# Performance work log

Measured on AMD Instinct MI355X. Metric: run time of the kernel, lower is better.

The kernel has to match this reference:

```python
import jax, jax.numpy as jnp
import numpy as np

N_NODES = 20000
N_GRAPH = 256
NODE_DIM = 128
MULS = (128, 64, 32)       # node irreps: 128x0e + 64x1o + 32x2e
HC = 32                    # hidden channels per irrep
HIDDEN_DIM = 64
N_PATH = 9                 # feasible uuw paths into 0e+1e+2e
W_NUMEL = N_PATH * HC * HC # 9216


def _tables():
    # real Clebsch-Gordan tensors built from cartesian tensor algebra,
    # normalized so that sum(C**2) = 2*l_out + 1 (component normalization)
    eps = np.zeros((3, 3, 3))
    eps[0, 1, 2] = eps[1, 2, 0] = eps[2, 0, 1] = 1.0
    eps[0, 2, 1] = eps[2, 1, 0] = eps[1, 0, 2] = -1.0
    s2, s6 = 1 / np.sqrt(2), 1 / np.sqrt(6)
    Q2 = np.zeros((5, 3, 3))  # orthonormal basis of traceless symmetric 3x3
    Q2[0, 0, 1] = Q2[0, 1, 0] = s2          # xy
    Q2[1, 1, 2] = Q2[1, 2, 1] = s2          # yz
    Q2[2, 0, 0] = Q2[2, 1, 1] = -s6; Q2[2, 2, 2] = 2 * s6  # z2
    Q2[3, 0, 2] = Q2[3, 2, 0] = s2          # xz
    Q2[4, 0, 0] = s2; Q2[4, 1, 1] = -s2     # x2-y2

    def nrm(C, l3):
        return C * np.sqrt((2 * l3 + 1) / (C ** 2).sum())

    C000 = np.ones((1, 1, 1))
    C022 = np.eye(5)[None, :, :]
    C110 = np.eye(3).reshape(3, 3, 1) / np.sqrt(3)
    C111 = eps / np.sqrt(2)
    C112 = np.transpose(Q2, (1, 2, 0))
    C202 = np.eye(5)[:, None, :]
    C220 = np.eye(5).reshape(5, 5, 1) / np.sqrt(5)
    M = np.einsum('iab,jdb->ijad', Q2, Q2)  # [5,5,3,3]
    C221 = nrm(np.einsum('cad,ijad->ijc', eps, M), 1)
    S = 0.5 * (M + np.transpose(M, (0, 1, 3, 2)))
    S = S - np.trace(S, axis1=2, axis2=3)[..., None, None] * np.eye(3) / 3.0
    C222 = nrm(np.einsum('kad,ijad->ijk', Q2, S), 2)
    # sph2cart change of basis: 9 spherical comps (0e+1e+2e) -> 3x3 cartesian
    Qc = np.zeros((3, 3, 9))
    Qc[:, :, 0] = np.eye(3) / np.sqrt(3)        # isotropic part
    Qc[:, :, 1:4] = eps / np.sqrt(2)            # antisymmetric part
    Qc[:, :, 4:9] = np.transpose(Q2, (1, 2, 0)) # symmetric traceless part
    return [C000, C022, C110, C111, C112, C202, C220, C221, C222], Qc

_CGS, _QC = _tables()


def setup_inputs() -> dict:
    key = jax.random.key(0)
    ks = jax.random.split(key, 12)
    f32 = jnp.float32
    d_sph = MULS[0] + 3 * MULS[1] + 5 * MULS[2]  # 480
    return {
        'x_scalar': jax.random.normal(ks[0], (N_NODES, NODE_DIM), f32),
        'x_spherical': jax.random.normal(ks[1], (N_NODES, d_sph), f32),
        'batch': jnp.sort(jax.random.randint(ks[2], (N_NODES,), 0, N_GRAPH)),
        'W0e': jax.random.normal(ks[3], (MULS[0], HC), f32),
        'W1o': jax.random.normal(ks[4], (MULS[1], HC), f32),
        'W2e': jax.random.normal(ks[5], (MULS[2], HC), f32),
        'Wm1': jax.random.normal(ks[6], (NODE_DIM, HIDDEN_DIM), f32) / np.sqrt(NODE_DIM),
        'bm1': jnp.zeros((HIDDEN_DIM,), f32),
        'Wm2': jax.random.normal(ks[7], (HIDDEN_DIM, W_NUMEL), f32) / np.sqrt(HIDDEN_DIM),
        'bm2': jnp.zeros((W_NUMEL,), f32),
        'P0': jax.random.normal(ks[8], (3 * HC,), f32),
        'P1': jax.random.normal(ks[9], (2 * HC,), f32),
        'P2': jax.random.normal(ks[10], (4 * HC,), f32),
    }


def reference(x_scalar, x_spherical, batch, W0e, W1o, W2e, Wm1, bm1, Wm2, bm2, P0, P1, P2):
    n = x_scalar.shape[0]
    m0, m1, m2 = MULS
    # split node features into irrep blocks
    x0 = x_spherical[:, :m0, None]                        # [N,128,1] 0e
    x1 = x_spherical[:, m0:m0 + 3 * m1].reshape(n, m1, 3) # [N,64,3]  1o
    x2 = x_spherical[:, m0 + 3 * m1:].reshape(n, m2, 5)   # [N,32,5]  2e
    # pre_lin: per-irrep channel mixing (e3nn-style 1/sqrt(fan_in))
    h = [jnp.einsum('num,uv->nvm', x, W) / np.sqrt(W.shape[0])
         for x, W in ((x0, W0e), (x1, W1o), (x2, W2e))]   # each [N,32,2l+1]
    # per-node tensor-product weights from scalar features
    w = (jax.nn.silu(x_scalar @ Wm1 + bm1) @ Wm2 + bm2).reshape(n, N_PATH, HC, HC)
    # uuw tensor product, path order matches _CGS
    paths = ((0, 0), (0, 2), (1, 1), (1, 1), (1, 1), (2, 0), (2, 2), (2, 2), (2, 2))
    inv_u = 1.0 / np.sqrt(HC)
    outs = []
    for k, (i, j) in enumerate(paths):
        C = jnp.asarray(_CGS[k], x_scalar.dtype)
        outs.append(jnp.einsum('pqr,nup,nuq,nuw->nwr', C, h[i], h[j], w[:, k]) * inv_u)
    # post_lin: combine paths of each output l into a single channel
    y0 = jnp.einsum('num,u->nm', jnp.concatenate([outs[0], outs[2], outs[6]], 1), P0) / np.sqrt(3 * HC)
    y1 = jnp.einsum('num,u->nm', jnp.concatenate([outs[3], outs[7]], 1), P1) / np.sqrt(2 * HC)
    y2 = jnp.einsum('num,u->nm', jnp.concatenate([outs[1], outs[4], outs[5], outs[8]], 1), P2) / np.sqrt(4 * HC)
    sph = jnp.concatenate([y0, y1, y2], axis=1)           # [N,9]
    cart = jnp.einsum('abi,ni->nab', jnp.asarray(_QC, sph.dtype), sph)  # [N,3,3]
    red = jax.ops.segment_sum(cart, batch, num_segments=N_GRAPH)        # [B,3,3]
    # if_trace is False (if_iso=False): roll every non-batch dim by 1
    return jnp.roll(jnp.roll(red, 1, axis=1), 1, axis=2)
```

## Files before the change

### kernel.cpp

```cpp
#include <hip/hip_runtime.h>
#include <math.h>

#define OFF_W2P 0
#define OFF_B2P 14336
#define OFF_V   14592
#define OFF_H0  4494592
#define OFF_H1  5134592
#define OFF_H2  7054592
#define WS_FLOATS 10254592

#define SC_Y0 0.0180421959121758f
#define SC_Y2 0.015625f
#define S2f 0.70710678118654752f
#define S6f 0.40824829046386302f
#define TWOS2f 1.41421356237309505f
#define TWOS6f 0.81649658092772603f
#define ISQRT3 0.57735026918962576f
#define ISQRT5 0.44721359549995794f
#define H0SC 0.08838834764831845f
#define H1SC 0.125f
#define H2SC 0.17677669529663689f

__device__ __constant__ int KARR[7] = {0, 1, 2, 4, 5, 6, 8};

__global__ __launch_bounds__(256) void prep_kernel(
    const float* __restrict__ Wm2, const float* __restrict__ bm2,
    const float* __restrict__ P0, const float* __restrict__ P2,
    float* __restrict__ ws, float* __restrict__ out) {
  int j = blockIdx.x * 256 + threadIdx.x;
  if (j < 2304) out[j] = 0.f;

  if (j < 14336) {
    int s = j >> 11; int rem = j & 2047; int c = rem >> 5; int u = rem & 31;
    int k = KARR[s];
    const float* P;
    float sc;
    switch (s) {
      case 0: P = P0;      sc = SC_Y0; break;
      case 1: P = P2;      sc = SC_Y2; break;
      case 2: P = P0 + 32; sc = SC_Y0; break;
      case 3: P = P2 + 32; sc = SC_Y2; break;
      case 4: P = P2 + 64; sc = SC_Y2; break;
      case 5: P = P0 + 64; sc = SC_Y0; break;
      default: P = P2 + 96; sc = SC_Y2; break;
    }
    const float4* w4 = (const float4*)(Wm2 + c * 9216 + k * 1024 + u * 32);
    const float4* p4 = (const float4*)P;
    float acc = 0.f;
#pragma unroll
    for (int q = 0; q < 8; ++q) {
      float4 a = w4[q], b = p4[q];
      acc += a.x * b.x + a.y * b.y + a.z * b.z + a.w * b.w;
    }
    ws[OFF_W2P + c * 224 + s * 32 + u] = acc * sc;
  } else if (j < 14560) {
    int i = j - 14336; int s = i >> 5; int u = i & 31; int k = KARR[s];
    const float* P;
    float sc;
    switch (s) {
      case 0: P = P0;      sc = SC_Y0; break;
      case 1: P = P2;      sc = SC_Y2; break;
      case 2: P = P0 + 32; sc = SC_Y0; break;
      case 3: P = P2 + 32; sc = SC_Y2; break;
      case 4: P = P2 + 64; sc = SC_Y2; break;
      case 5: P = P0 + 64; sc = SC_Y0; break;
      default: P = P2 + 96; sc = SC_Y2; break;
    }
    const float* b = bm2 + k * 1024 + u * 32;
    float acc = 0.f;
#pragma unroll
    for (int w = 0; w < 32; ++w) acc += b[w] * P[w];
    ws[OFF_B2P + s * 32 + u] = acc * sc;
  }
}

__global__ __launch_bounds__(256, 1) void kbc_kernel(
    const float* __restrict__ xs_g, const float* __restrict__ xsph,
    const float* __restrict__ W0e, const float* __restrict__ W1o,
    const float* __restrict__ W2e,
    const float* __restrict__ Wm1, const float* __restrict__ bm1,
    float* __restrict__ ws) {
  __shared__ __align__(16) char smem[30976];
  const int tid = threadIdx.x;

  if (blockIdx.x < 625) {
    float (*xs)[132] = (float (*)[132])smem;
    float (*hiT)[36] = (float (*)[36])(smem + 16896);
    const int n0 = blockIdx.x * 32;

    for (int idx = tid; idx < 1024; idx += 256) {
      const int row = idx >> 5, c4 = idx & 31;
      *(float4*)&xs[row][c4 * 4] = *(const float4*)(xs_g + (n0 + row) * 128 + c4 * 4);
    }
    __syncthreads();

    {
      const int cg = tid & 15, ng = tid >> 4;
      const int c0 = cg * 4, nl = ng * 2;
      float acc[2][4] = {{0.f}};
#pragma unroll 4
      for (int mq = 0; mq < 32; ++mq) {
        float4 xv[2];
        xv[0] = *(float4*)&xs[nl][mq * 4];
        xv[1] = *(float4*)&xs[nl + 1][mq * 4];
        float4 wv[4];
#pragma unroll
        for (int r = 0; r < 4; ++r) wv[r] = *(const float4*)(Wm1 + (mq * 4 + r) * 64 + c0);
#pragma unroll
        for (int r = 0; r < 4; ++r) {
          const float4 w = wv[r];
#pragma unroll
          for (int i = 0; i < 2; ++i) {
            const float xr = (r == 0) ? xv[i].x : (r == 1) ? xv[i].y : (r == 2) ? xv[i].z : xv[i].w;
            acc[i][0] += xr * w.x; acc[i][1] += xr * w.y;
            acc[i][2] += xr * w.z; acc[i][3] += xr * w.w;
          }
        }
      }
      const float4 bb = *(const float4*)(bm1 + c0);
#pragma unroll
      for (int jj = 0; jj < 4; ++jj) {
        float zz[2];
#pragma unroll
        for (int i = 0; i < 2; ++i) {
          float z = acc[i][jj] + ((jj == 0) ? bb.x : (jj == 1) ? bb.y : (jj == 2) ? bb.z : bb.w);
          zz[i] = z / (1.f + __expf(-z));
        }
        *(float2*)&hiT[c0 + jj][nl] = make_float2(zz[0], zz[1]);
      }
    }
    __syncthreads();

    if (tid < 224) {
      const int og = tid >> 3, ng = tid & 7;
      const int o0 = og * 8, nl = ng * 4;
      const float4 blo = *(const float4*)(ws + OFF_B2P + o0);
      const float4 bhi = *(const float4*)(ws + OFF_B2P + o0 + 4);
      float acc[4][8];
#pragma unroll
      for (int i = 0; i < 4; ++i) {
        acc[i][0] = blo.x; acc[i][1] = blo.y; acc[i][2] = blo.z; acc[i][3] = blo.w;
        acc[i][4] = bhi.x; acc[i][5] = bhi.y; acc[i][6] = bhi.z; acc[i][7] = bhi.w;
      }
#pragma unroll 2
      for (int c = 0; c < 64; ++c) {
        const float4 hv = *(float4*)&hiT[c][nl];
        const float4 wlo = *(const float4*)(ws + OFF_W2P + c * 224 + o0);
        const float4 whi = *(const float4*)(ws + OFF_W2P + c * 224 + o0 + 4);
        const float hvv[4] = {hv.x, hv.y, hv.z, hv.w};
        const float wv[8] = {wlo.x, wlo.y, wlo.z, wlo.w, whi.x, whi.y, whi.z, whi.w};
#pragma unroll
        for (int i = 0; i < 4; ++i)
#pragma unroll
          for (int jj = 0; jj < 8; ++jj) acc[i][jj] += hvv[i] * wv[jj];
      }
#pragma unroll
      for (int i = 0; i < 4; ++i) {
        const int n = n0 + nl + i;
        float4 a = {acc[i][0], acc[i][1], acc[i][2], acc[i][3]};
        float4 b = {acc[i][4], acc[i][5], acc[i][6], acc[i][7]};
        *(float4*)(ws + OFF_V + n * 224 + o0) = a;
        *(float4*)(ws + OFF_V + n * 224 + o0 + 4) = b;
      }
    }
  } else {
    float (*xp)[484] = (float (*)[484])smem;
    const int n0 = (blockIdx.x - 625) * 16;

    for (int idx = tid; idx < 1920; idx += 256) {
      const int row = idx / 120, c4 = idx % 120;
      *(float4*)&xp[row][c4 * 4] = *(const float4*)(xsph + (size_t)(n0 + row) * 480 + c4 * 4);
    }
    __syncthreads();

    if (tid < 64) {
      const int n = tid & 15, ug = tid >> 4;
      const int u0 = ug * 8;
      float acc[8] = {0.f};
#pragma unroll 4
      for (int mq = 0; mq < 32; ++mq) {
        const float4 xv = *(float4*)&xp[n][mq * 4];
        const float xa[4] = {xv.x, xv.y, xv.z, xv.w};
#pragma unroll
        for (int r = 0; r < 4; ++r) {
          const float4 wl = *(const float4*)(W0e + (mq * 4 + r) * 32 + u0);
          const float4 wh = *(const float4*)(W0e + (mq * 4 + r) * 32 + u0 + 4);
          const float xr = xa[r];
          acc[0] += xr * wl.x; acc[1] += xr * wl.y; acc[2] += xr * wl.z; acc[3] += xr * wl.w;
          acc[4] += xr * wh.x; acc[5] += xr * wh.y; acc[6] += xr * wh.z; acc[7] += xr * wh.w;
        }
      }
      const int n_g = n0 + n;
      float4 a = {acc[0] * H0SC, acc[1] * H0SC, acc[2] * H0SC, acc[3] * H0SC};
      float4 b = {acc[4] * H0SC, acc[5] * H0SC, acc[6] * H0SC, acc[7] * H0SC};
      *(float4*)(ws + OFF_H0 + n_g * 32 + u0) = a;
      *(float4*)(ws + OFF_H0 + n_g * 32 + u0 + 4) = b;
    } else if (tid < 128) {
      const int t = tid - 64;
      const int n = t & 15, ug = t >> 4;
      const int u0 = ug * 8;
      float acc[3][8] = {{0.f}};
#pragma unroll 2
      for (int mq = 0; mq < 16; ++mq) {
        const float4 a0 = *(float4*)&xp[n][128 + mq * 12];
        const float4 a1 = *(float4*)&xp[n][128 + mq * 12 + 4];
        const float4 a2 = *(float4*)&xp[n][128 + mq * 12 + 8];
        const float xa[12] = {a0.x, a0.y, a0.z, a0.w, a1.x, a1.y, a1.z, a1.w,
                              a2.x, a2.y, a2.z, a2.w};
#pragma unroll
        for (int mm = 0; mm < 4; ++mm) {
          const float4 wl = *(const float4*)(W1o + (mq * 4 + mm) * 32 + u0);
          const float4 wh = *(const float4*)(W1o + (mq * 4 + mm) * 32 + u0 + 4);
          const float wv[8] = {wl.x, wl.y, wl.z, wl.w, wh.x, wh.y, wh.z, wh.w};
#pragma unroll
          for (int j = 0; j < 3; ++j) {
            const float xr = xa[mm * 3 + j];
#pragma unroll
            for (int jj = 0; jj < 8; ++jj) acc[j][jj] += xr * wv[jj];
          }
        }
      }
      const int n_g = n0 + n;
#pragma unroll
      for (int j = 0; j < 3; ++j) {
        float4 a = {acc[j][0] * H1SC, acc[j][1] * H1SC, acc[j][2] * H1SC, acc[j][3] * H1SC};
        float4 b = {acc[j][4] * H1SC, acc[j][5] * H1SC, acc[j][6] * H1SC, acc[j][7] * H1SC};
        *(float4*)(ws + OFF_H1 + (n_g * 3 + j) * 32 + u0) = a;
        *(float4*)(ws + OFF_H1 + (n_g * 3 + j) * 32 + u0 + 4) = b;
      }
    } else if (tid < 192) {
      const int t = tid - 128;
      const int n = t & 15, ug = t >> 4;
      const int u0 = ug * 8;
      float acc[5][8] = {{0.f}};
#pragma unroll 2
      for (int mq = 0; mq < 8; ++mq) {
        const float4 a0 = *(float4*)&xp[n][320 + mq * 20];
        const float4 a1 = *(float4*)&xp[n][320 + mq * 20 + 4];
        const float4 a2 = *(float4*)&xp[n][320 + mq * 20 + 8];
        const float4 a3 = *(float4*)&xp[n][320 + mq * 20 + 12];
        const float4 a4 = *(float4*)&xp[n][320 + mq * 20 + 16];
        const float xa[20] = {a0.x, a0.y, a0.z, a0.w, a1.x, a1.y, a1.z, a1.w,
                              a2.x, a2.y, a2.z, a2.w, a3.x, a3.y, a3.z, a3.w,
                              a4.x, a4.y, a4.z, a4.w};
#pragma unroll
        for (int mm = 0; mm < 4; ++mm) {
          const float4 wl = *(const float4*)(W2e + (mq * 4 + mm) * 32 + u0);
          const float4 wh = *(const float4*)(W2e + (mq * 4 + mm) * 32 + u0 + 4);
          const float wv[8] = {wl.x, wl.y, wl.z, wl.w, wh.x, wh.y, wh.z, wh.w};
#pragma unroll
          for (int j = 0; j < 5; ++j) {
            const float xr = xa[mm * 5 + j];
#pragma unroll
            for (int jj = 0; jj < 8; ++jj) acc[j][jj] += xr * wv[jj];
          }
        }
      }
      const int n_g = n0 + n;
#pragma unroll
      for (int j = 0; j < 5; ++j) {
        float4 a = {acc[j][0] * H2SC, acc[j][1] * H2SC, acc[j][2] * H2SC, acc[j][3] * H2SC};
        float4 b = {acc[j][4] * H2SC, acc[j][5] * H2SC, acc[j][6] * H2SC, acc[j][7] * H2SC};
        *(float4*)(ws + OFF_H2 + (n_g * 5 + j) * 32 + u0) = a;
        *(float4*)(ws + OFF_H2 + (n_g * 5 + j) * 32 + u0 + 4) = b;
      }
    }
  }
}

__global__ __launch_bounds__(256) void kd_kernel(
    const float* __restrict__ ws, const int* __restrict__ batch,
    float* __restrict__ out, const float norm2) {
  const int tid = threadIdx.x;
  const int nl = tid >> 5, un = tid & 31;
  const int n0 = blockIdx.x * 8;
  const int n = n0 + nl;

  const float* V = ws + OFF_V + n * 224 + un;
  const float v0 = V[0], v1 = V[32], v2 = V[64], v3 = V[96];
  const float v4 = V[128], v5 = V[160], v6 = V[192];
  const float h0 = ws[OFF_H0 + n * 32 + un];
  const float h1a = ws[OFF_H1 + (n * 3 + 0) * 32 + un];
  const float h1b = ws[OFF_H1 + (n * 3 + 1) * 32 + un];
  const float h1c = ws[OFF_H1 + (n * 3 + 2) * 32 + un];
  float h2v[5];
#pragma unroll
  for (int j = 0; j < 5; ++j) h2v[j] = ws[OFF_H2 + (n * 5 + j) * 32 + un];

  const float d11 = h1a * h1a + h1b * h1b + h1c * h1c;
  const float d22 = h2v[0] * h2v[0] + h2v[1] * h2v[1] + h2v[2] * h2v[2] +
                    h2v[3] * h2v[3] + h2v[4] * h2v[4];
  float y0 = v0 * h0 * h0 + v2 * d11 * ISQRT3 + v5 * d22 * ISQRT5;

  const float o00 = h1a * h1a, o01 = h1a * h1b, o02 = h1a * h1c;
  const float o11 = h1b * h1b, o12 = h1b * h1c, o22 = h1c * h1c;
  const float t40 = TWOS2f * o01, t41 = TWOS2f * o12;
  const float t42 = S6f * (2.f * o22 - o00 - o11);
  const float t43 = TWOS2f * o02, t44 = S2f * (o00 - o11);

  const float A00 = -S6f * h2v[2] + S2f * h2v[4];
  const float A01 = S2f * h2v[0];
  const float A02 = S2f * h2v[3];
  const float A11 = -S6f * h2v[2] - S2f * h2v[4];
  const float A12 = S2f * h2v[1];
  const float A22 = TWOS6f * h2v[2];
  const float B00 = A00 * A00 + A01 * A01 + A02 * A02;
  const float B01 = A00 * A01 + A01 * A11 + A02 * A12;
  const float B02 = A00 * A02 + A01 * A12 + A02 * A22;
  const float B11 = A01 * A01 + A11 * A11 + A12 * A12;
  const float B12 = A01 * A02 + A11 * A12 + A12 * A22;
  const float B22 = A02 * A02 + A12 * A12 + A22 * A22;
  const float t80 = TWOS2f * B01, t81 = TWOS2f * B12;
  const float t82 = S6f * (2.f * B22 - B00 - B11);
  const float t83 = TWOS2f * B02, t84 = S2f * (B00 - B11);

  const float w15 = (v1 + v4) * h0;
  const float v6n = v6 * norm2;
  float y2r[5];
  y2r[0] = w15 * h2v[0] + v3 * t40 + v6n * t80;
  y2r[1] = w15 * h2v[1] + v3 * t41 + v6n * t81;
  y2r[2] = w15 * h2v[2] + v3 * t42 + v6n * t82;
  y2r[3] = w15 * h2v[3] + v3 * t43 + v6n * t83;
  y2r[4] = w15 * h2v[4] + v3 * t44 + v6n * t84;

#pragma unroll
  for (int off = 16; off > 0; off >>= 1) {
    y0 += __shfl_xor(y0, off, 32);
#pragma unroll
    for (int r = 0; r < 5; ++r) y2r[r] += __shfl_xor(y2r[r], off, 32);
  }

  __shared__ float sphs[8][6];
  if (un == 0) {
    sphs[nl][0] = y0;
#pragma unroll
    for (int r = 0; r < 5; ++r) sphs[nl][1 + r] = y2r[r];
  }
  __syncthreads();

  if (tid < 9) {
    const float QW[9][6] = {
        {ISQRT3, 0.f, 0.f, -S6f, 0.f, S2f},
        {0.f, S2f, 0.f, 0.f, 0.f, 0.f},
        {0.f, 0.f, 0.f, 0.f, S2f, 0.f},
        {0.f, S2f, 0.f, 0.f, 0.f, 0.f},
        {ISQRT3, 0.f, 0.f, -S6f, 0.f, -S2f},
        {0.f, 0.f, S2f, 0.f, 0.f, 0.f},
        {0.f, 0.f, 0.f, 0.f, S2f, 0.f},
        {0.f, 0.f, S2f, 0.f, 0.f, 0.f},
        {ISQRT3, 0.f, 0.f, TWOS6f, 0.f, 0.f}};
    const int a = tid / 3, b = tid % 3;
    const int rolled = ((a + 1) % 3) * 3 + ((b + 1) % 3);
    const float c0 = QW[tid][0], c1 = QW[tid][1], c2 = QW[tid][2];
    const float c3 = QW[tid][3], c4 = QW[tid][4], c5 = QW[tid][5];
    int cur_g = batch[n0];
    float acc = 0.f;
#pragma unroll
    for (int q = 0; q < 8; ++q) {
      const int g = batch[n0 + q];
      const float val = c0 * sphs[q][0] + c1 * sphs[q][1] + c2 * sphs[q][2] +
                        c3 * sphs[q][3] + c4 * sphs[q][4] + c5 * sphs[q][5];
      if (g != cur_g) {
        atomicAdd(out + cur_g * 9 + rolled, acc);
        acc = 0.f;
        cur_g = g;
      }
      acc += val;
    }
    atomicAdd(out + cur_g * 9 + rolled, acc);
  }
}

extern "C" void kernel_launch(void* const* d_in, const int* in_sizes, int n_in,
                              void* d_out, int out_size, void* d_ws, size_t ws_size,
                              hipStream_t stream) {
  const float* x_scalar = (const float*)d_in[0];
  const float* x_sph    = (const float*)d_in[1];
  const int*   batch    = (const int*)d_in[2];
  const float* W0e      = (const float*)d_in[3];
  const float* W1o      = (const float*)d_in[4];
  const float* W2e      = (const float*)d_in[5];
  const float* Wm1      = (const float*)d_in[6];
  const float* bm1      = (const float*)d_in[7];
  const float* Wm2      = (const float*)d_in[8];
  const float* bm2      = (const float*)d_in[9];
  const float* P0       = (const float*)d_in[10];
  const float* P2       = (const float*)d_in[12];
  float* ws  = (float*)d_ws;
  float* out = (float*)d_out;

  if (ws_size < (size_t)WS_FLOATS * sizeof(float)) return;

  double Q2[5][3][3] = {};
  const double s2d = 0.70710678118654752440, s6d = 0.40824829046386301637;
  Q2[0][0][1] = Q2[0][1][0] = s2d;
  Q2[1][1][2] = Q2[1][2][1] = s2d;
  Q2[2][0][0] = Q2[2][1][1] = -s6d; Q2[2][2][2] = 2.0 * s6d;
  Q2[3][0][2] = Q2[3][2][0] = s2d;
  Q2[4][0][0] = s2d; Q2[4][1][1] = -s2d;
  double ss = 0.0;
  for (int i = 0; i < 5; ++i)
    for (int jj = 0; jj < 5; ++jj) {
      double S[3][3];
      for (int a = 0; a < 3; ++a)
        for (int d = 0; d < 3; ++d) {
          double m1 = 0, m2 = 0;
          for (int b = 0; b < 3; ++b) {
            m1 += Q2[i][a][b] * Q2[jj][d][b];
            m2 += Q2[i][d][b] * Q2[jj][a][b];
          }
          S[a][d] = 0.5 * (m1 + m2);
        }
      double tr = (S[0][0] + S[1][1] + S[2][2]) / 3.0;
      S[0][0] -= tr; S[1][1] -= tr; S[2][2] -= tr;
      for (int kk = 0; kk < 5; ++kk) {
        double cc = 0;
        for (int a = 0; a < 3; ++a)
          for (int d = 0; d < 3; ++d) cc += Q2[kk][a][d] * S[a][d];
        ss += cc * cc;
      }
    }
  const float norm2 = (float)sqrt(5.0 / ss);

  prep_kernel<<<57, 256, 0, stream>>>(Wm2, bm2, P0, P2, ws, out);
  kbc_kernel<<<1875, 256, 0, stream>>>(x_scalar, x_sph, W0e, W1o, W2e, Wm1, bm1, ws);
  kd_kernel<<<2500, 256, 0, stream>>>(ws, batch, out, norm2);
}
```

Baseline: 157.0 us.

## Fuse projection, weight MLP and tensor-product reduction into one kernel

Merges the node-projection/MLP kernel and the tensor-product/segment-sum kernel into a single kernel that processes 16 nodes per block. The per-node V, h0, h1 and h2 intermediates now stay in shared memory and registers instead of being written to and re-read from a large global workspace. This removes that HBM round trip and one kernel launch. In exchange each block uses about 50 KB of shared memory and must do all stages serially, and the work per stage is split differently across threads (e.g. one output channel per thread for the h projections), which may lower per-stage efficiency or occupancy.

```diff
diff --git a/kernel.cpp b/kernel.cpp
--- a/kernel.cpp
+++ b/kernel.cpp
@@ -3,11 +3,7 @@
 
 #define OFF_W2P 0
 #define OFF_B2P 14336
-#define OFF_V   14592
-#define OFF_H0  4494592
-#define OFF_H1  5134592
-#define OFF_H2  7054592
-#define WS_FLOATS 10254592
+#define WS_FLOATS 14592
 
 #define SC_Y0 0.0180421959121758f
 #define SC_Y2 0.015625f
@@ -74,267 +70,227 @@
   }
 }
 
-__global__ __launch_bounds__(256, 1) void kbc_kernel(
+__global__ __launch_bounds__(256, 3) void fused_kernel(
     const float* __restrict__ xs_g, const float* __restrict__ xsph,
     const float* __restrict__ W0e, const float* __restrict__ W1o,
     const float* __restrict__ W2e,
     const float* __restrict__ Wm1, const float* __restrict__ bm1,
-    float* __restrict__ ws) {
-  __shared__ __align__(16) char smem[30976];
-  const int tid = threadIdx.x;
-
-  if (blockIdx.x < 625) {
-    float (*xs)[132] = (float (*)[132])smem;
-    float (*hiT)[36] = (float (*)[36])(smem + 16896);
-    const int n0 = blockIdx.x * 32;
-
-    for (int idx = tid; idx < 1024; idx += 256) {
-      const int row = idx >> 5, c4 = idx & 31;
-      *(float4*)&xs[row][c4 * 4] = *(const float4*)(xs_g + (n0 + row) * 128 + c4 * 4);
-    }
-    __syncthreads();
-
-    {
-      const int cg = tid & 15, ng = tid >> 4;
-      const int c0 = cg * 4, nl = ng * 2;
-      float acc[2][4] = {{0.f}};
-#pragma unroll 4
-      for (int mq = 0; mq < 32; ++mq) {
-        float4 xv[2];
-        xv[0] = *(float4*)&xs[nl][mq * 4];
-        xv[1] = *(float4*)&xs[nl + 1][mq * 4];
-        float4 wv[4];
-#pragma unroll
-        for (int r = 0; r < 4; ++r) wv[r] = *(const float4*)(Wm1 + (mq * 4 + r) * 64 + c0);
-#pragma unroll
-        for (int r = 0; r < 4; ++r) {
-          const float4 w = wv[r];
-#pragma unroll
-          for (int i = 0; i < 2; ++i) {
-            const float xr = (r == 0) ? xv[i].x : (r == 1) ? xv[i].y : (r == 2) ? xv[i].z : xv[i].w;
-            acc[i][0] += xr * w.x; acc[i][1] += xr * w.y;
-            acc[i][2] += xr * w.z; acc[i][3] += xr * w.w;
-          }
-        }
-      }
-      const float4 bb = *(const float4*)(bm1 + c0);
-#pragma unroll
-      for (int jj = 0; jj < 4; ++jj) {
-        float zz[2];
-#pragma unroll
-        for (int i = 0; i < 2; ++i) {
-          float z = acc[i][jj] + ((jj == 0) ? bb.x : (jj == 1) ? bb.y : (jj == 2) ? bb.z : bb.w);
-          zz[i] = z / (1.f + __expf(-z));
-        }
-        *(float2*)&hiT[c0 + jj][nl] = make_float2(zz[0], zz[1]);
-      }
-    }
-    __syncthreads();
-
-    if (tid < 224) {
-      const int og = tid >> 3, ng = tid & 7;
-      const int o0 = og * 8, nl = ng * 4;
-      const float4 blo = *(const float4*)(ws + OFF_B2P + o0);
-      const float4 bhi = *(const float4*)(ws + OFF_B2P + o0 + 4);
-      float acc[4][8];
-#pragma unroll
-      for (int i = 0; i < 4; ++i) {
-        acc[i][0] = blo.x; acc[i][1] = blo.y; acc[i][2] = blo.z; acc[i][3] = blo.w;
-        acc[i][4] = bhi.x; acc[i][5] = bhi.y; acc[i][6] = bhi.z; acc[i][7] = bhi.w;
-      }
-#pragma unroll 2
-      for (int c = 0; c < 64; ++c) {
-        const float4 hv = *(float4*)&hiT[c][nl];
-        const float4 wlo = *(const float4*)(ws + OFF_W2P + c * 224 + o0);
-        const float4 whi = *(const float4*)(ws + OFF_W2P + c * 224 + o0 + 4);
-        const float hvv[4] = {hv.x, hv.y, hv.z, hv.w};
-        const float wv[8] = {wlo.x, wlo.y, wlo.z, wlo.w, whi.x, whi.y, whi.z, whi.w};
-#pragma unroll
-        for (int i = 0; i < 4; ++i)
-#pragma unroll
-          for (int jj = 0; jj < 8; ++jj) acc[i][jj] += hvv[i] * wv[jj];
-      }
-#pragma unroll
-      for (int i = 0; i < 4; ++i) {
-        const int n = n0 + nl + i;
-        float4 a = {acc[i][0], acc[i][1], acc[i][2], acc[i][3]};
-        float4 b = {acc[i][4], acc[i][5], acc[i][6], acc[i][7]};
-        *(float4*)(ws + OFF_V + n * 224 + o0) = a;
-        *(float4*)(ws + OFF_V + n * 224 + o0 + 4) = b;
-      }
-    }
-  } else {
-    float (*xp)[484] = (float (*)[484])smem;
-    const int n0 = (blockIdx.x - 625) * 16;
-
-    for (int idx = tid; idx < 1920; idx += 256) {
-      const int row = idx / 120, c4 = idx % 120;
-      *(float4*)&xp[row][c4 * 4] = *(const float4*)(xsph + (size_t)(n0 + row) * 480 + c4 * 4);
-    }
-    __syncthreads();
-
-    if (tid < 64) {
-      const int n = tid & 15, ug = tid >> 4;
-      const int u0 = ug * 8;
-      float acc[8] = {0.f};
-#pragma unroll 4
-      for (int mq = 0; mq < 32; ++mq) {
-        const float4 xv = *(float4*)&xp[n][mq * 4];
-        const float xa[4] = {xv.x, xv.y, xv.z, xv.w};
-#pragma unroll
-        for (int r = 0; r < 4; ++r) {
-          const float4 wl = *(const float4*)(W0e + (mq * 4 + r) * 32 + u0);
-          const float4 wh = *(const float4*)(W0e + (mq * 4 + r) * 32 + u0 + 4);
-          const float xr = xa[r];
-          acc[0] += xr * wl.x; acc[1] += xr * wl.y; acc[2] += xr * wl.z; acc[3] += xr * wl.w;
-          acc[4] += xr * wh.x; acc[5] += xr * wh.y; acc[6] += xr * wh.z; acc[7] += xr * wh.w;
-        }
-      }
-      const int n_g = n0 + n;
-      float4 a = {acc[0] * H0SC, acc[1] * H0SC, acc[2] * H0SC, acc[3] * H0SC};
-      float4 b = {acc[4] * H0SC, acc[5] * H0SC, acc[6] * H0SC, acc[7] * H0SC};
-      *(float4*)(ws + OFF_H0 + n_g * 32 + u0) = a;
-      *(float4*)(ws + OFF_H0 + n_g * 32 + u0 + 4) = b;
-    } else if (tid < 128) {
-      const int t = tid - 64;
-      const int n = t & 15, ug = t >> 4;
-      const int u0 = ug * 8;
-      float acc[3][8] = {{0.f}};
-#pragma unroll 2
-      for (int mq = 0; mq < 16; ++mq) {
-        const float4 a0 = *(float4*)&xp[n][128 + mq * 12];
-        const float4 a1 = *(float4*)&xp[n][128 + mq * 12 + 4];
-        const float4 a2 = *(float4*)&xp[n][128 + mq * 12 + 8];
-        const float xa[12] = {a0.x, a0.y, a0.z, a0.w, a1.x, a1.y, a1.z, a1.w,
-                              a2.x, a2.y, a2.z, a2.w};
-#pragma unroll
-        for (int mm = 0; mm < 4; ++mm) {
-          const float4 wl = *(const float4*)(W1o + (mq * 4 + mm) * 32 + u0);
-          const float4 wh = *(const float4*)(W1o + (mq * 4 + mm) * 32 + u0 + 4);
-          const float wv[8] = {wl.x, wl.y, wl.z, wl.w, wh.x, wh.y, wh.z, wh.w};
-#pragma unroll
-          for (int j = 0; j < 3; ++j) {
-            const float xr = xa[mm * 3 + j];
-#pragma unroll
-            for (int jj = 0; jj < 8; ++jj) acc[j][jj] += xr * wv[jj];
-          }
-        }
-      }
-      const int n_g = n0 + n;
-#pragma unroll
-      for (int j = 0; j < 3; ++j) {
-        float4 a = {acc[j][0] * H1SC, acc[j][1] * H1SC, acc[j][2] * H1SC, acc[j][3] * H1SC};
-        float4 b = {acc[j][4] * H1SC, acc[j][5] * H1SC, acc[j][6] * H1SC, acc[j][7] * H1SC};
-        *(float4*)(ws + OFF_H1 + (n_g * 3 + j) * 32 + u0) = a;
-        *(float4*)(ws + OFF_H1 + (n_g * 3 + j) * 32 + u0 + 4) = b;
-      }
-    } else if (tid < 192) {
-      const int t = tid - 128;
-      const int n = t & 15, ug = t >> 4;
-      const int u0 = ug * 8;
-      float acc[5][8] = {{0.f}};
-#pragma unroll 2
-      for (int mq = 0; mq < 8; ++mq) {
-        const float4 a0 = *(float4*)&xp[n][320 + mq * 20];
-        const float4 a1 = *(float4*)&xp[n][320 + mq * 20 + 4];
-        const float4 a2 = *(float4*)&xp[n][320 + mq * 20 + 8];
-        const float4 a3 = *(float4*)&xp[n][320 + mq * 20 + 12];
-        const float4 a4 = *(float4*)&xp[n][320 + mq * 20 + 16];
-        const float xa[20] = {a0.x, a0.y, a0.z, a0.w, a1.x, a1.y, a1.z, a1.w,
-                              a2.x, a2.y, a2.z, a2.w, a3.x, a3.y, a3.z, a3.w,
-                              a4.x, a4.y, a4.z, a4.w};
-#pragma unroll
-        for (int mm = 0; mm < 4; ++mm) {
-          const float4 wl = *(const float4*)(W2e + (mq * 4 + mm) * 32 + u0);
-          const float4 wh = *(const float4*)(W2e + (mq * 4 + mm) * 32 + u0 + 4);
-          const float wv[8] = {wl.x, wl.y, wl.z, wl.w, wh.x, wh.y, wh.z, wh.w};
-#pragma unroll
-          for (int j = 0; j < 5; ++j) {
-            const float xr = xa[mm * 5 + j];
-#pragma unroll
-            for (int jj = 0; jj < 8; ++jj) acc[j][jj] += xr * wv[jj];
-          }
-        }
-      }
-      const int n_g = n0 + n;
-#pragma unroll
-      for (int j = 0; j < 5; ++j) {
-        float4 a = {acc[j][0] * H2SC, acc[j][1] * H2SC, acc[j][2] * H2SC, acc[j][3] * H2SC};
-        float4 b = {acc[j][4] * H2SC, acc[j][5] * H2SC, acc[j][6] * H2SC, acc[j][7] * H2SC};
-        *(float4*)(ws + OFF_H2 + (n_g * 5 + j) * 32 + u0) = a;
-        *(float4*)(ws + OFF_H2 + (n_g * 5 + j) * 32 + u0 + 4) = b;
-      }
-    }
-  }
-}
-
-__global__ __launch_bounds__(256) void kd_kernel(
     const float* __restrict__ ws, const int* __restrict__ batch,
     float* __restrict__ out, const float norm2) {
+  __shared__ __align__(16) char smem[50560];
+  float (*xs)[132] = (float (*)[132])smem;
+  float (*Vt)[228] = (float (*)[228])smem;
+  float (*xp)[484] = (float (*)[484])(smem + 14592);
+  float (*hiT)[18] = (float (*)[18])(smem + 45568);
+  float (*sphs)[6] = (float (*)[6])(smem + 50176);
+
   const int tid = threadIdx.x;
-  const int nl = tid >> 5, un = tid & 31;
-  const int n0 = blockIdx.x * 8;
-  const int n = n0 + nl;
-
-  const float* V = ws + OFF_V + n * 224 + un;
-  const float v0 = V[0], v1 = V[32], v2 = V[64], v3 = V[96];
-  const float v4 = V[128], v5 = V[160], v6 = V[192];
-  const float h0 = ws[OFF_H0 + n * 32 + un];
-  const float h1a = ws[OFF_H1 + (n * 3 + 0) * 32 + un];
-  const float h1b = ws[OFF_H1 + (n * 3 + 1) * 32 + un];
-  const float h1c = ws[OFF_H1 + (n * 3 + 2) * 32 + un];
-  float h2v[5];
-#pragma unroll
-  for (int j = 0; j < 5; ++j) h2v[j] = ws[OFF_H2 + (n * 5 + j) * 32 + un];
-
-  const float d11 = h1a * h1a + h1b * h1b + h1c * h1c;
-  const float d22 = h2v[0] * h2v[0] + h2v[1] * h2v[1] + h2v[2] * h2v[2] +
-                    h2v[3] * h2v[3] + h2v[4] * h2v[4];
-  float y0 = v0 * h0 * h0 + v2 * d11 * ISQRT3 + v5 * d22 * ISQRT5;
-
-  const float o00 = h1a * h1a, o01 = h1a * h1b, o02 = h1a * h1c;
-  const float o11 = h1b * h1b, o12 = h1b * h1c, o22 = h1c * h1c;
-  const float t40 = TWOS2f * o01, t41 = TWOS2f * o12;
-  const float t42 = S6f * (2.f * o22 - o00 - o11);
-  const float t43 = TWOS2f * o02, t44 = S2f * (o00 - o11);
-
-  const float A00 = -S6f * h2v[2] + S2f * h2v[4];
-  const float A01 = S2f * h2v[0];
-  const float A02 = S2f * h2v[3];
-  const float A11 = -S6f * h2v[2] - S2f * h2v[4];
-  const float A12 = S2f * h2v[1];
-  const float A22 = TWOS6f * h2v[2];
-  const float B00 = A00 * A00 + A01 * A01 + A02 * A02;
-  const float B01 = A00 * A01 + A01 * A11 + A02 * A12;
-  const float B02 = A00 * A02 + A01 * A12 + A02 * A22;
-  const float B11 = A01 * A01 + A11 * A11 + A12 * A12;
-  const float B12 = A01 * A02 + A11 * A12 + A12 * A22;
-  const float B22 = A02 * A02 + A12 * A12 + A22 * A22;
-  const float t80 = TWOS2f * B01, t81 = TWOS2f * B12;
-  const float t82 = S6f * (2.f * B22 - B00 - B11);
-  const float t83 = TWOS2f * B02, t84 = S2f * (B00 - B11);
-
-  const float w15 = (v1 + v4) * h0;
-  const float v6n = v6 * norm2;
-  float y2r[5];
-  y2r[0] = w15 * h2v[0] + v3 * t40 + v6n * t80;
-  y2r[1] = w15 * h2v[1] + v3 * t41 + v6n * t81;
-  y2r[2] = w15 * h2v[2] + v3 * t42 + v6n * t82;
-  y2r[3] = w15 * h2v[3] + v3 * t43 + v6n * t83;
-  y2r[4] = w15 * h2v[4] + v3 * t44 + v6n * t84;
-
-#pragma unroll
-  for (int off = 16; off > 0; off >>= 1) {
-    y0 += __shfl_xor(y0, off, 32);
-#pragma unroll
-    for (int r = 0; r < 5; ++r) y2r[r] += __shfl_xor(y2r[r], off, 32);
-  }
-
-  __shared__ float sphs[8][6];
-  if (un == 0) {
-    sphs[nl][0] = y0;
-#pragma unroll
-    for (int r = 0; r < 5; ++r) sphs[nl][1 + r] = y2r[r];
+  const int n0 = blockIdx.x * 16;
+
+  for (int idx = tid; idx < 512; idx += 256) {
+    const int row = idx >> 5, c4 = idx & 31;
+    *(float4*)&xs[row][c4 * 4] = *(const float4*)(xs_g + (size_t)(n0 + row) * 128 + c4 * 4);
+  }
+  for (int idx = tid; idx < 1920; idx += 256) {
+    const int row = idx / 120, c4 = idx % 120;
+    *(float4*)&xp[row][c4 * 4] = *(const float4*)(xsph + (size_t)(n0 + row) * 480 + c4 * 4);
+  }
+  __syncthreads();
+
+  {
+    const int n = tid >> 4, c0 = (tid & 15) * 4;
+    float acc[4] = {0.f, 0.f, 0.f, 0.f};
+#pragma unroll 4
+    for (int mq = 0; mq < 32; ++mq) {
+      const float4 xv = *(float4*)&xs[n][mq * 4];
+      const float xa[4] = {xv.x, xv.y, xv.z, xv.w};
+#pragma unroll
+      for (int r = 0; r < 4; ++r) {
+        const float4 w = *(const float4*)(Wm1 + (mq * 4 + r) * 64 + c0);
+        const float xr = xa[r];
+        acc[0] += xr * w.x; acc[1] += xr * w.y;
+        acc[2] += xr * w.z; acc[3] += xr * w.w;
+      }
+    }
+    const float4 bb = *(const float4*)(bm1 + c0);
+    const float ba[4] = {bb.x, bb.y, bb.z, bb.w};
+#pragma unroll
+    for (int jj = 0; jj < 4; ++jj) {
+      const float z = acc[jj] + ba[jj];
+      hiT[c0 + jj][n] = z / (1.f + __expf(-z));
+    }
+  }
+  __syncthreads();
+
+  if (tid < 224) {
+    const int og = tid >> 3, ng = tid & 7;
+    const int o0 = og * 8, nl = ng * 2;
+    const float4 blo = *(const float4*)(ws + OFF_B2P + o0);
+    const float4 bhi = *(const float4*)(ws + OFF_B2P + o0 + 4);
+    float acc[2][8];
+#pragma unroll
+    for (int i = 0; i < 2; ++i) {
+      acc[i][0] = blo.x; acc[i][1] = blo.y; acc[i][2] = blo.z; acc[i][3] = blo.w;
+      acc[i][4] = bhi.x; acc[i][5] = bhi.y; acc[i][6] = bhi.z; acc[i][7] = bhi.w;
+    }
+#pragma unroll 2
+    for (int c = 0; c < 64; ++c) {
+      const float2 hv = *(float2*)&hiT[c][nl];
+      const float4 wlo = *(const float4*)(ws + OFF_W2P + c * 224 + o0);
+      const float4 whi = *(const float4*)(ws + OFF_W2P + c * 224 + o0 + 4);
+      const float hvv[2] = {hv.x, hv.y};
+      const float wv[8] = {wlo.x, wlo.y, wlo.z, wlo.w, whi.x, whi.y, whi.z, whi.w};
+#pragma unroll
+      for (int i = 0; i < 2; ++i)
+#pragma unroll
+        for (int jj = 0; jj < 8; ++jj) acc[i][jj] += hvv[i] * wv[jj];
+    }
+#pragma unroll
+    for (int i = 0; i < 2; ++i) {
+      float4 a = {acc[i][0], acc[i][1], acc[i][2], acc[i][3]};
+      float4 b = {acc[i][4], acc[i][5], acc[i][6], acc[i][7]};
+      *(float4*)&Vt[nl + i][o0] = a;
+      *(float4*)&Vt[nl + i][o0 + 4] = b;
+    }
+  }
+  __syncthreads();
+
+  const int u = tid & 31, ni = tid >> 5;
+
+  float h0v[2] = {0.f, 0.f};
+#pragma unroll 4
+  for (int mq = 0; mq < 32; ++mq) {
+    const float4 va = *(float4*)&xp[ni][mq * 4];
+    const float4 vb = *(float4*)&xp[ni + 8][mq * 4];
+    const float xa[4] = {va.x, va.y, va.z, va.w};
+    const float xb[4] = {vb.x, vb.y, vb.z, vb.w};
+#pragma unroll
+    for (int r = 0; r < 4; ++r) {
+      const float w = W0e[(mq * 4 + r) * 32 + u];
+      h0v[0] += xa[r] * w;
+      h0v[1] += xb[r] * w;
+    }
+  }
+  h0v[0] *= H0SC; h0v[1] *= H0SC;
+
+  float h1v[2][3] = {{0.f, 0.f, 0.f}, {0.f, 0.f, 0.f}};
+#pragma unroll 2
+  for (int mq = 0; mq < 16; ++mq) {
+    const float4 a0 = *(float4*)&xp[ni][128 + mq * 12];
+    const float4 a1 = *(float4*)&xp[ni][128 + mq * 12 + 4];
+    const float4 a2 = *(float4*)&xp[ni][128 + mq * 12 + 8];
+    const float4 b0 = *(float4*)&xp[ni + 8][128 + mq * 12];
+    const float4 b1 = *(float4*)&xp[ni + 8][128 + mq * 12 + 4];
+    const float4 b2 = *(float4*)&xp[ni + 8][128 + mq * 12 + 8];
+    const float xa[12] = {a0.x, a0.y, a0.z, a0.w, a1.x, a1.y, a1.z, a1.w,
+                          a2.x, a2.y, a2.z, a2.w};
+    const float xb[12] = {b0.x, b0.y, b0.z, b0.w, b1.x, b1.y, b1.z, b1.w,
+                          b2.x, b2.y, b2.z, b2.w};
+#pragma unroll
+    for (int mm = 0; mm < 4; ++mm) {
+      const float w = W1o[(mq * 4 + mm) * 32 + u];
+#pragma unroll
+      for (int j = 0; j < 3; ++j) {
+        h1v[0][j] += xa[mm * 3 + j] * w;
+        h1v[1][j] += xb[mm * 3 + j] * w;
+      }
+    }
+  }
+#pragma unroll
+  for (int j = 0; j < 3; ++j) { h1v[0][j] *= H1SC; h1v[1][j] *= H1SC; }
+
+  float h2r[2][5] = {{0.f, 0.f, 0.f, 0.f, 0.f}, {0.f, 0.f, 0.f, 0.f, 0.f}};
+#pragma unroll 2
+  for (int mq = 0; mq < 8; ++mq) {
+    const float4 a0 = *(float4*)&xp[ni][320 + mq * 20];
+    const float4 a1 = *(float4*)&xp[ni][320 + mq * 20 + 4];
+    const float4 a2 = *(float4*)&xp[ni][320 + mq * 20 + 8];
+    const float4 a3 = *(float4*)&xp[ni][320 + mq * 20 + 12];
+    const float4 a4 = *(float4*)&xp[ni][320 + mq * 20 + 16];
+    const float4 b0 = *(float4*)&xp[ni + 8][320 + mq * 20];
+    const float4 b1 = *(float4*)&xp[ni + 8][320 + mq * 20 + 4];
+    const float4 b2 = *(float4*)&xp[ni + 8][320 + mq * 20 + 8];
+    const float4 b3 = *(float4*)&xp[ni + 8][320 + mq * 20 + 12];
+    const float4 b4 = *(float4*)&xp[ni + 8][320 + mq * 20 + 16];
+    const float xa[20] = {a0.x, a0.y, a0.z, a0.w, a1.x, a1.y, a1.z, a1.w,
+                          a2.x, a2.y, a2.z, a2.w, a3.x, a3.y, a3.z, a3.w,
+                          a4.x, a4.y, a4.z, a4.w};
+    const float xb[20] = {b0.x, b0.y, b0.z, b0.w, b1.x, b1.y, b1.z, b1.w,
+                          b2.x, b2.y, b2.z, b2.w, b3.x, b3.y, b3.z, b3.w,
+                          b4.x, b4.y, b4.z, b4.w};
+#pragma unroll
+    for (int mm = 0; mm < 4; ++mm) {
+      const float w = W2e[(mq * 4 + mm) * 32 + u];
+#pragma unroll
+      for (int j = 0; j < 5; ++j) {
+        h2r[0][j] += xa[mm * 5 + j] * w;
+        h2r[1][j] += xb[mm * 5 + j] * w;
+      }
+    }
+  }
+#pragma unroll
+  for (int j = 0; j < 5; ++j) { h2r[0][j] *= H2SC; h2r[1][j] *= H2SC; }
+
+#pragma unroll
+  for (int it = 0; it < 2; ++it) {
+    const int ln = ni + 8 * it;
+    const float* Vp = &Vt[ln][u];
+    const float v0 = Vp[0], v1 = Vp[32], v2 = Vp[64], v3 = Vp[96];
+    const float v4 = Vp[128], v5 = Vp[160], v6 = Vp[192];
+    const float h0 = h0v[it];
+    const float h1a = h1v[it][0], h1b = h1v[it][1], h1c = h1v[it][2];
+    float h2v[5];
+#pragma unroll
+    for (int j = 0; j < 5; ++j) h2v[j] = h2r[it][j];
+
+    const float d11 = h1a * h1a + h1b * h1b + h1c * h1c;
+    const float d22 = h2v[0] * h2v[0] + h2v[1] * h2v[1] + h2v[2] * h2v[2] +
+                      h2v[3] * h2v[3] + h2v[4] * h2v[4];
+    float y0 = v0 * h0 * h0 + v2 * d11 * ISQRT3 + v5 * d22 * ISQRT5;
+
+    const float o00 = h1a * h1a, o01 = h1a * h1b, o02 = h1a * h1c;
+    const float o11 = h1b * h1b, o12 = h1b * h1c, o22 = h1c * h1c;
+    const float t40 = TWOS2f * o01, t41 = TWOS2f * o12;
+    const float t42 = S6f * (2.f * o22 - o00 - o11);
+    const float t43 = TWOS2f * o02, t44 = S2f * (o00 - o11);
+
+    const float A00 = -S6f * h2v[2] + S2f * h2v[4];
+    const float A01 = S2f * h2v[0];
+    const float A02 = S2f * h2v[3];
+    const float A11 = -S6f * h2v[2] - S2f * h2v[4];
+    const float A12 = S2f * h2v[1];
+    const float A22 = TWOS6f * h2v[2];
+    const float B00 = A00 * A00 + A01 * A01 + A02 * A02;
+    const float B01 = A00 * A01 + A01 * A11 + A02 * A12;
+    const float B02 = A00 * A02 + A01 * A12 + A02 * A22;
+    const float B11 = A01 * A01 + A11 * A11 + A12 * A12;
+    const float B12 = A01 * A02 + A11 * A12 + A12 * A22;
+    const float B22 = A02 * A02 + A12 * A12 + A22 * A22;
+    const float t80 = TWOS2f * B01, t81 = TWOS2f * B12;
+    const float t82 = S6f * (2.f * B22 - B00 - B11);
+    const float t83 = TWOS2f * B02, t84 = S2f * (B00 - B11);
+
+    const float w15 = (v1 + v4) * h0;
+    const float v6n = v6 * norm2;
+    float y2r[5];
+    y2r[0] = w15 * h2v[0] + v3 * t40 + v6n * t80;
+    y2r[1] = w15 * h2v[1] + v3 * t41 + v6n * t81;
+    y2r[2] = w15 * h2v[2] + v3 * t42 + v6n * t82;
+    y2r[3] = w15 * h2v[3] + v3 * t43 + v6n * t83;
+    y2r[4] = w15 * h2v[4] + v3 * t44 + v6n * t84;
+
+#pragma unroll
+    for (int off = 16; off > 0; off >>= 1) {
+      y0 += __shfl_xor(y0, off, 32);
+#pragma unroll
+      for (int r = 0; r < 5; ++r) y2r[r] += __shfl_xor(y2r[r], off, 32);
+    }
+
+    if (u == 0) {
+      sphs[ln][0] = y0;
+#pragma unroll
+      for (int r = 0; r < 5; ++r) sphs[ln][1 + r] = y2r[r];
+    }
   }
   __syncthreads();
 
@@ -356,7 +312,7 @@
     int cur_g = batch[n0];
     float acc = 0.f;
 #pragma unroll
-    for (int q = 0; q < 8; ++q) {
+    for (int q = 0; q < 16; ++q) {
       const int g = batch[n0 + q];
       const float val = c0 * sphs[q][0] + c1 * sphs[q][1] + c2 * sphs[q][2] +
                         c3 * sphs[q][3] + c4 * sphs[q][4] + c5 * sphs[q][5];
@@ -423,6 +379,6 @@
   const float norm2 = (float)sqrt(5.0 / ss);
 
   prep_kernel<<<57, 256, 0, stream>>>(Wm2, bm2, P0, P2, ws, out);
-  kbc_kernel<<<1875, 256, 0, stream>>>(x_scalar, x_sph, W0e, W1o, W2e, Wm1, bm1, ws);
-  kd_kernel<<<2500, 256, 0, stream>>>(ws, batch, out, norm2);
+  fused_kernel<<<1250, 256, 0, stream>>>(x_scalar, x_sph, W0e, W1o, W2e,
+                                         Wm1, bm1, ws, batch, out, norm2);
 }
```

New measurement: 162.3 us. +3.4%, slower.
